# Kernel optimization log

Hardware: AMD Instinct MI355X
Metric: run time of the kernel (lower is better)

Reference implementation:

```python
import jax, jax.numpy as jnp
import numpy as np
from jax import lax

T, B = 80, 32
ACT, CIN, HID, LSTM_H = 16, 4, 512, 256

def _conv(x, w, b, stride, pad):
    y = lax.conv_general_dilated(x, w, (stride, stride), [(pad, pad), (pad, pad)],
                                 dimension_numbers=('NCHW', 'OIHW', 'NCHW'))
    return y + b[None, :, None, None]

def setup_inputs() -> dict:
    key = jax.random.key(0)
    ks = jax.random.split(key, 20)
    s = 0.02
    return {
        'x': jax.random.uniform(ks[0], (T, B, CIN, 84, 84), dtype=jnp.float32),
        'last_action': jax.random.randint(ks[1], (T, B), 0, ACT),
        'reward': jax.random.normal(ks[2], (T, B), dtype=jnp.float32),
        'dones': jnp.zeros((T, B), dtype=bool),
        'hx': jax.random.normal(ks[3], (2, B, LSTM_H), dtype=jnp.float32) * s,
        'conv1_w': jax.random.normal(ks[4], (32, CIN, 8, 8), jnp.float32) * s,
        'conv1_b': jnp.zeros((32,), jnp.float32),
        'conv2_w': jax.random.normal(ks[5], (64, 32, 4, 4), jnp.float32) * s,
        'conv2_b': jnp.zeros((64,), jnp.float32),
        'conv3_w': jax.random.normal(ks[6], (64, 64, 3, 3), jnp.float32) * s,
        'conv3_b': jnp.zeros((64,), jnp.float32),
        'fc_w': jax.random.normal(ks[7], (HID, 3136), jnp.float32) * s,
        'fc_b': jnp.zeros((HID,), jnp.float32),
        'lstm_wih': jax.random.normal(ks[8], (4 * LSTM_H, HID + ACT + 1), jnp.float32) * s,
        'lstm_whh': jax.random.normal(ks[9], (4 * LSTM_H, LSTM_H), jnp.float32) * s,
        'lstm_bih': jnp.zeros((4 * LSTM_H,), jnp.float32),
        'lstm_bhh': jnp.zeros((4 * LSTM_H,), jnp.float32),
        'actor_w': jax.random.normal(ks[10], (ACT, LSTM_H), jnp.float32) * s,
        'actor_b': jnp.zeros((ACT,), jnp.float32),
        'critic_w': jax.random.normal(ks[11], (1, LSTM_H), jnp.float32) * s,
        'critic_b': jnp.zeros((1,), jnp.float32),
    }

def reference(x, last_action, reward, dones, hx,
              conv1_w, conv1_b, conv2_w, conv2_b, conv3_w, conv3_b,
              fc_w, fc_b, lstm_wih, lstm_whh, lstm_bih, lstm_bhh,
              actor_w, actor_b, critic_w, critic_b):
    seq_len, bs = x.shape[0], x.shape[1]
    xf = x.reshape(seq_len * bs, CIN, 84, 84)          # combine time & batch
    la = jax.nn.one_hot(last_action.reshape(-1), ACT, dtype=jnp.float32)
    rw = reward.reshape(-1, 1)

    lrelu = lambda v: jax.nn.leaky_relu(v, 0.01)
    h = lrelu(_conv(xf, conv1_w, conv1_b, 4, 1))       # [N,32,20,20]
    h = lrelu(_conv(h, conv2_w, conv2_b, 2, 0))        # [N,64,9,9]
    h = lrelu(_conv(h, conv3_w, conv3_b, 1, 0))        # [N,64,7,7]
    h = h.reshape(h.shape[0], -1)                      # [N,3136]
    h = lrelu(h @ fc_w.T + fc_b)                       # [N,512]
    h = jnp.concatenate([h, rw, la], axis=1)           # [N,529]
    h = h.reshape(seq_len, bs, -1)

    def step(carry, inp):
        xt, dt = inp                                   # [bs,529], [bs] bool
        carry = jnp.where(dt[None, :, None], 0.0, carry)
        hh, cc = carry[0], carry[1]
        gates = xt @ lstm_wih.T + lstm_bih + hh @ lstm_whh.T + lstm_bhh
        i, f, g, o = jnp.split(gates, 4, axis=1)
        cc = jax.nn.sigmoid(f) * cc + jax.nn.sigmoid(i) * jnp.tanh(g)
        hh = jax.nn.sigmoid(o) * jnp.tanh(cc)
        return jnp.stack([hh, cc], 0), hh

    _, hs = lax.scan(step, hx, (h, dones))             # hs: [T,bs,256]
    feat = hs.reshape(seq_len * bs, LSTM_H)

    logits = feat @ actor_w.T + actor_b                # [N,16]
    values = feat @ critic_w.T + critic_b              # [N,1]
    logits = jnp.where(jnp.isnan(logits), jnp.float32(1e-12), logits)
    return logits.reshape(seq_len, -1, bs), values.reshape(seq_len, bs)
```

## Files before the change

kernel.cpp:

```cpp
#include <hip/hip_runtime.h>
#include <math.h>

#define T_ 80
#define B_ 32
#define N_ 2560
#define LH_ 256

typedef __attribute__((ext_vector_type(8))) short short8;
typedef __attribute__((ext_vector_type(4))) float f32x4;
#define MFMA16(a, b, c) __builtin_amdgcn_mfma_f32_16x16x32_bf16((a), (b), (c), 0, 0, 0)

__device__ __forceinline__ float lrelu(float v) { return v > 0.f ? v : 0.01f * v; }
__device__ __forceinline__ short f2bf(float f) {
    unsigned u = __float_as_uint(f);
    return (short)((u + 0x7fffu + ((u >> 16) & 1u)) >> 16);
}

__global__ void pack_all_k(const float* __restrict__ c1w, const float* __restrict__ c2w,
                           const float* __restrict__ c3w, const float* __restrict__ fcw,
                           const float* __restrict__ wih,
                           short* __restrict__ wp1, short* __restrict__ wp2,
                           short* __restrict__ wp3, short* __restrict__ wfcP,
                           short* __restrict__ wihP, int* __restrict__ cnt) {
    __shared__ short rowb[3136];
    int blk = blockIdx.x, tidx = threadIdx.x;
    if (blk < 512) {
        int j = blk;
        for (int i = tidx; i < 3136; i += 256) rowb[i] = f2bf(fcw[j * 3136 + i]);
        __syncthreads();
        for (int i = tidx; i < 3136; i += 256) {
            int p = i >> 6, oc = i & 63;
            wfcP[j * 3136 + i] = rowb[oc * 49 + p];
        }
        return;
    }
    blk -= 512;
    if (blk < 2048) {
        int g = blk * 256 + tidx;
        int r = g >> 9, k = g & 511;
        wihP[g] = f2bf(wih[r * 529 + k]);
        return;
    }
    blk -= 2048;
    if (blk < 32) {
        int g = blk * 256 + tidx;
        int ky = g >> 10, oc = (g >> 5) & 31, k = g & 31, kx = k >> 2, ci = k & 3;
        wp1[g] = f2bf(c1w[((oc * 4 + ci) * 8 + ky) * 8 + kx]);
        return;
    }
    blk -= 32;
    if (blk < 128) {
        int g = blk * 256 + tidx;
        int t = g >> 11, oc = (g >> 5) & 63, ci = g & 31, ky = t >> 2, kx = t & 3;
        wp2[g] = f2bf(c2w[((oc * 32 + ci) * 4 + ky) * 4 + kx]);
        return;
    }
    blk -= 128;
    if (blk < 144) {
        int g = blk * 256 + tidx;
        int tkc = g >> 11, oc = (g >> 5) & 63, c32 = g & 31;
        int t = tkc >> 1, kc = tkc & 1, ky = t / 3, kx = t % 3;
        wp3[g] = f2bf(c3w[((oc * 64 + kc * 32 + c32) * 3 + ky) * 3 + kx]);
        return;
    }
    cnt[tidx] = 0; cnt[256 + tidx] = 0;
}

#define C1_RS 344
__global__ __launch_bounds__(512) void conv123_mfma(
    const float* __restrict__ x,
    const short* __restrict__ wp1, const float* __restrict__ b1v,
    const short* __restrict__ wp2, const float* __restrict__ b2v,
    const short* __restrict__ wp3, const float* __restrict__ b3v,
    short* __restrict__ h3) {
    __shared__ short xs[44 * C1_RS];
    __shared__ short h1s[400 * 40];
    __shared__ short ob2[96 * 72];
    int n = blockIdx.x, tid = threadIdx.x;
    int lane = tid & 63, wid = tid >> 6;
    int lr = lane & 15, kq = lane >> 4;

    short8 bfr1[8][2];
#pragma unroll
    for (int ky = 0; ky < 8; ++ky)
#pragma unroll
        for (int nt = 0; nt < 2; ++nt)
            bfr1[ky][nt] = *(const short8*)&wp1[((ky * 32) + nt * 16 + lr) * 32 + kq * 8];
    float b0 = b1v[lr], b1 = b1v[16 + lr];

#pragma unroll
    for (int pass = 0; pass < 2; ++pass) {
        const int iybase = pass ? 39 : -1;
        for (int i = tid; i < 44 * 84; i += 512) {
            int ry = i / 84, xi4 = i % 84;
            int ci = xi4 / 21, x4 = xi4 % 21;
            int iy = iybase + ry;
            if (iy < 0) continue;
            float4 v = *(const float4*)(x + (size_t)(n * 4 + ci) * 7056 + iy * 84 + x4 * 4);
            int base = ry * C1_RS + (x4 * 4 + 1) * 4 + ci;
            xs[base] = f2bf(v.x); xs[base + 4] = f2bf(v.y);
            xs[base + 8] = f2bf(v.z); xs[base + 12] = f2bf(v.w);
        }
        for (int i = tid; i < 44 * 4; i += 512)
            xs[(i >> 2) * C1_RS + (i & 3)] = 0;
        if (pass == 0)
            for (int i = tid; i < C1_RS; i += 512) xs[i] = 0;
        __syncthreads();

        for (int t = wid; t < 13; t += 8) {
            int pl = t * 16 + lr; if (pl > 199) pl = 199;
            int p = pass * 200 + pl;
            int oy = p / 20, ox = p % 20;
            f32x4 acc0 = {0.f, 0.f, 0.f, 0.f}, acc1 = {0.f, 0.f, 0.f, 0.f};
#pragma unroll
            for (int ky = 0; ky < 8; ++ky) {
                int ry = oy * 4 + ky - (pass ? 40 : 0);
                short8 af = *(const short8*)&xs[ry * C1_RS + ox * 16 + kq * 8];
                acc0 = MFMA16(af, bfr1[ky][0], acc0);
                acc1 = MFMA16(af, bfr1[ky][1], acc1);
            }
#pragma unroll
            for (int r = 0; r < 4; ++r) {
                int rp = t * 16 + kq * 4 + r;
                if (rp < 200) {
                    int row = pass * 200 + rp;
                    h1s[row * 40 + lr]      = f2bf(lrelu(acc0[r] + b0));
                    h1s[row * 40 + 16 + lr] = f2bf(lrelu(acc1[r] + b1));
                }
            }
        }
        __syncthreads();
    }

    int nt = wid & 3, mh = wid >> 2;
    {
        short8 bfr[16];
#pragma unroll
        for (int t = 0; t < 16; ++t)
            bfr[t] = *(const short8*)&wp2[(t * 64 + nt * 16 + lr) * 32 + kq * 8];
        float bl = b2v[nt * 16 + lr];
        for (int mt = mh * 3; mt < mh * 3 + 3; ++mt) {
            int p = mt * 16 + lr; if (p > 80) p = 80;
            int oy = p / 9, ox = p % 9;
            f32x4 acc = {0.f, 0.f, 0.f, 0.f};
#pragma unroll
            for (int ky = 0; ky < 4; ++ky)
#pragma unroll
                for (int kx = 0; kx < 4; ++kx) {
                    int pix = (oy * 2 + ky) * 20 + ox * 2 + kx;
                    short8 af = *(const short8*)&h1s[pix * 40 + kq * 8];
                    acc = MFMA16(af, bfr[ky * 4 + kx], acc);
                }
            int pm = mt * 16 + kq * 4;
#pragma unroll
            for (int r = 0; r < 4; ++r)
                ob2[(pm + r) * 72 + nt * 16 + lr] = f2bf(lrelu(acc[r] + bl));
        }
    }
    __syncthreads();
    {
        short8 cfr[18];
#pragma unroll
        for (int t = 0; t < 18; ++t)
            cfr[t] = *(const short8*)&wp3[(t * 64 + nt * 16 + lr) * 32 + kq * 8];
        float bl3 = b3v[nt * 16 + lr];
        short* ob3 = xs;
        for (int mt = mh * 2; mt < mh * 2 + 2; ++mt) {
            int p = mt * 16 + lr; if (p > 48) p = 48;
            int oy = p / 7, ox = p % 7;
            f32x4 acc = {0.f, 0.f, 0.f, 0.f};
#pragma unroll
            for (int ky = 0; ky < 3; ++ky)
#pragma unroll
                for (int kx = 0; kx < 3; ++kx) {
                    int pix = (oy + ky) * 9 + ox + kx;
#pragma unroll
                    for (int kc = 0; kc < 2; ++kc) {
                        short8 af = *(const short8*)&ob2[pix * 72 + kc * 32 + kq * 8];
                        acc = MFMA16(af, cfr[(ky * 3 + kx) * 2 + kc], acc);
                    }
                }
            int pm = mt * 16 + kq * 4;
#pragma unroll
            for (int r = 0; r < 4; ++r)
                ob3[(pm + r) * 64 + nt * 16 + lr] = f2bf(lrelu(acc[r] + bl3));
        }
    }
    __syncthreads();
    uint4* dst = (uint4*)(h3 + (size_t)n * 3136);
    for (int i = tid; i < 392; i += 512) dst[i] = ((uint4*)xs)[i];
}

template <int OUT>
__global__ __launch_bounds__(256) void gemm_bf16(
    const short* __restrict__ A, const short* __restrict__ B,
    const float* __restrict__ bias, void* __restrict__ Cout,
    int M, int N, int K, int ldc,
    const float* __restrict__ reward = nullptr, const int* __restrict__ la = nullptr,
    const float* __restrict__ wih = nullptr, const float* __restrict__ bih = nullptr,
    const float* __restrict__ bhh = nullptr) {
    __shared__ short smem[15360];
    int m0 = blockIdx.y * 128, n0 = blockIdx.x * 64;
    int tid = threadIdx.x;
    int lane = tid & 63, wid = tid >> 6;
    int wr = wid >> 1, wc = wid & 1;
    int lr = lane & 15, kq = lane >> 4;
    f32x4 acc[4][2];
#pragma unroll
    for (int i = 0; i < 4; ++i)
#pragma unroll
        for (int j = 0; j < 2; ++j) acc[i][j] = (f32x4){0.f, 0.f, 0.f, 0.f};

    int nsteps = K >> 5;
#define STAGE(k0, buf)                                                          \
    {                                                                           \
        short* As = smem + (buf) * 5120;                                        \
        short* Bs = smem + 10240 + (buf) * 2560;                                \
        for (int i = tid; i < 512; i += 256) {                                  \
            int row = i >> 2, c4 = i & 3;                                       \
            *(uint4*)&As[row * 40 + c4 * 8] =                                   \
                *(const uint4*)&A[(size_t)(m0 + row) * K + (k0) + c4 * 8];      \
        }                                                                       \
        {                                                                       \
            int row = tid >> 2, c4 = tid & 3;                                   \
            *(uint4*)&Bs[row * 40 + c4 * 8] =                                   \
                *(const uint4*)&B[(size_t)(n0 + row) * K + (k0) + c4 * 8];      \
        }                                                                       \
    }
    STAGE(0, 0);
    __syncthreads();
    for (int ks = 0; ks < nsteps; ++ks) {
        int buf = ks & 1;
        if (ks + 1 < nsteps) STAGE((ks + 1) * 32, buf ^ 1);
        short* As = smem + buf * 5120;
        short* Bs = smem + 10240 + buf * 2560;
        short8 af[4], bfr[2];
#pragma unroll
        for (int i = 0; i < 4; ++i)
            af[i] = *(const short8*)&As[(wr * 64 + i * 16 + lr) * 40 + kq * 8];
#pragma unroll
        for (int j = 0; j < 2; ++j)
            bfr[j] = *(const short8*)&Bs[(wc * 32 + j * 16 + lr) * 40 + kq * 8];
#pragma unroll
        for (int i = 0; i < 4; ++i)
#pragma unroll
            for (int j = 0; j < 2; ++j)
                acc[i][j] = MFMA16(af[i], bfr[j], acc[i][j]);
        __syncthreads();
    }
#undef STAGE
    if (OUT == 2) {
        float* C = (float*)Cout;
#pragma unroll
        for (int i = 0; i < 4; ++i)
#pragma unroll
            for (int j = 0; j < 2; ++j) {
                int col = n0 + wc * 32 + j * 16 + lr;
                const float* wrow = wih + (size_t)col * 529;
                float base = bih[col] + bhh[col];
                float w512 = wrow[512];
#pragma unroll
                for (int r = 0; r < 4; ++r) {
                    int row = m0 + wr * 64 + i * 16 + kq * 4 + r;
                    C[(size_t)row * ldc + col] =
                        acc[i][j][r] + base + reward[row] * w512 + wrow[513 + la[row]];
                }
            }
    } else {
        short* ob = smem;
#pragma unroll
        for (int i = 0; i < 4; ++i)
#pragma unroll
            for (int j = 0; j < 2; ++j) {
                int col = wc * 32 + j * 16 + lr;
                float bl = bias[n0 + col];
#pragma unroll
                for (int r = 0; r < 4; ++r) {
                    int row = wr * 64 + i * 16 + kq * 4 + r;
                    ob[row * 64 + col] = f2bf(lrelu(acc[i][j][r] + bl));
                }
            }
        __syncthreads();
        short* C = (short*)Cout;
        for (int i = tid; i < 1024; i += 256) {
            int row = i >> 3, c8 = i & 7;
            *(uint4*)&C[(size_t)(m0 + row) * ldc + n0 + c8 * 8] =
                *(uint4*)&ob[row * 64 + c8 * 8];
        }
    }
}

__global__ __launch_bounds__(512) void lstm16_k(
    const float* __restrict__ gx,
    const float* __restrict__ whh,
    const unsigned char* __restrict__ dones,
    const float* __restrict__ hx,
    float* __restrict__ hs,
    unsigned short* __restrict__ hpub,
    int* __restrict__ cnt) {
    const int tid = threadIdx.x;
    const int grp  = blockIdx.x & 7;
    const int half = blockIdx.x >> 3;
    const int lane = tid & 63, w = tid >> 6;
    const int gt = w >> 1, s2 = w & 1;
    const int lr = lane & 15, kq = lane >> 4;

    __shared__ short hB[16 * 264];
    __shared__ float gate_s[4][128][4];

    short8 afr[4][8];
#pragma unroll
    for (int mi = 0; mi < 4; ++mi) {
        int row = gt * 256 + half * 128 + s2 * 64 + mi * 16 + lr;
        const float* wr = whh + (size_t)row * 256;
#pragma unroll
        for (int kt = 0; kt < 8; ++kt) {
            int k0 = kt * 32 + kq * 8;
            float4 a = *(const float4*)(wr + k0);
            float4 b = *(const float4*)(wr + k0 + 4);
            short8 f;
            f[0] = f2bf(a.x); f[1] = f2bf(a.y); f[2] = f2bf(a.z); f[3] = f2bf(a.w);
            f[4] = f2bf(b.x); f[5] = f2bf(b.y); f[6] = f2bf(b.z); f[7] = f2bf(b.w);
            afr[mi][kt] = f;
        }
    }
    {
        int* ap = (int*)afr;
#pragma unroll
        for (int i = 0; i < 128; ++i) asm volatile("" : "+v"(ap[i]));
    }

    for (int i = tid; i < 12 * 264; i += 512) hB[4 * 264 + i] = 0;

    const int u = tid >> 2, bt = tid & 3;
    const int b = grp * 4 + bt, gu = half * 128 + u;
    float cc = hx[(size_t)B_ * LH_ + b * LH_ + gu];

#pragma unroll
    for (int l = 0; l < 2; ++l) {
        int e = tid + l * 512;
        int bt2 = e >> 8, k = e & 255;
        int b2 = grp * 4 + bt2;
        float hv = hx[b2 * LH_ + k];
        if (dones[b2]) hv = 0.f;
        hB[bt2 * 264 + k] = f2bf(hv);
    }
    __syncthreads();

    const int mycnt = (grp * 2 + half) * 32, peercnt = (grp * 2 + (half ^ 1)) * 32;
    const int phalf = (half ^ 1) << 7;

    for (int t = 1; t <= T_; ++t) {
        const int nb0 = (t - 1) * B_;
        float gxv[4];
#pragma unroll
        for (int g2 = 0; g2 < 4; ++g2)
            gxv[g2] = gx[(size_t)(nb0 + b) * 1024 + g2 * 256 + gu];

        if (t > 1) {
            if (tid == 0) {
                while (__hip_atomic_load(&cnt[peercnt], __ATOMIC_RELAXED,
                                         __HIP_MEMORY_SCOPE_AGENT) < t - 1) {}
                __builtin_amdgcn_fence(__ATOMIC_ACQUIRE, "agent");
            }
            __syncthreads();
            int bt2 = tid >> 7, pu = tid & 127;
            int b2 = grp * 4 + bt2, pgu = phalf + pu;
            hB[bt2 * 264 + pgu] =
                (short)hpub[((t - 1) & 1) * 8192 + b2 * 256 + pgu];
        }
        __syncthreads();

        f32x4 acc[4] = {{0.f,0.f,0.f,0.f},{0.f,0.f,0.f,0.f},
                        {0.f,0.f,0.f,0.f},{0.f,0.f,0.f,0.f}};
#pragma unroll
        for (int kt = 0; kt < 8; ++kt) {
            short8 bfr = *(const short8*)&hB[lr * 264 + kt * 32 + kq * 8];
#pragma unroll
            for (int mi = 0; mi < 4; ++mi)
                acc[mi] = MFMA16(afr[mi][kt], bfr, acc[mi]);
        }
        if (lr < 4) {
#pragma unroll
            for (int mi = 0; mi < 4; ++mi)
#pragma unroll
                for (int r = 0; r < 4; ++r)
                    gate_s[gt][s2 * 64 + mi * 16 + kq * 4 + r][lr] = acc[mi][r];
        }
        __syncthreads();

        {
            bool dn = dones[nb0 + b] != 0;
            float gi = gate_s[0][u][bt] + gxv[0];
            float gf = gate_s[1][u][bt] + gxv[1];
            float gg = gate_s[2][u][bt] + gxv[2];
            float go = gate_s[3][u][bt] + gxv[3];
            float ccv = dn ? 0.f : cc;
            float si = 1.f / (1.f + expf(-gi));
            float sf = 1.f / (1.f + expf(-gf));
            float so = 1.f / (1.f + expf(-go));
            float c2 = sf * ccv + si * tanhf(gg);
            float h2 = so * tanhf(c2);
            cc = c2;
            if (t < T_) {
                short hm = f2bf(dones[t * B_ + b] ? 0.f : h2);
                hpub[(t & 1) * 8192 + b * 256 + gu] = (unsigned short)hm;
                hB[bt * 264 + gu] = hm;
            }
            hs[(size_t)(nb0 + b) * LH_ + gu] = h2;
        }
        __syncthreads();
        if (tid == 0)
            __hip_atomic_store(&cnt[mycnt], t, __ATOMIC_RELEASE,
                               __HIP_MEMORY_SCOPE_AGENT);
    }
}

__global__ void head_k(const float* __restrict__ hs,
                       const float* __restrict__ aw, const float* __restrict__ ab,
                       const float* __restrict__ cw, const float* __restrict__ cb,
                       float* __restrict__ out) {
    int gid = blockIdx.x * 256 + threadIdx.x;
    if (gid >= N_ * 17) return;
    int n = gid / 17, r = gid % 17;
    const float* f = hs + (size_t)n * 256;
    if (r < 16) {
        const float* w = aw + r * 256;
        float acc = ab[r];
        for (int k = 0; k < 256; ++k) acc = fmaf(f[k], w[k], acc);
        if (isnan(acc)) acc = 1e-12f;
        out[(size_t)n * 16 + r] = acc;
    } else {
        float acc = cb[0];
        for (int k = 0; k < 256; ++k) acc = fmaf(f[k], cw[k], acc);
        out[(size_t)N_ * 16 + n] = acc;
    }
}

extern "C" void kernel_launch(void* const* d_in, const int* in_sizes, int n_in,
                              void* d_out, int out_size, void* d_ws, size_t ws_size,
                              hipStream_t stream) {
    const float* x      = (const float*)d_in[0];
    const int* la       = (const int*)d_in[1];
    const float* reward = (const float*)d_in[2];
    const unsigned char* dones = (const unsigned char*)d_in[3];
    const float* hx     = (const float*)d_in[4];
    const float* c1w = (const float*)d_in[5];  const float* c1b = (const float*)d_in[6];
    const float* c2w = (const float*)d_in[7];  const float* c2b = (const float*)d_in[8];
    const float* c3w = (const float*)d_in[9];  const float* c3b = (const float*)d_in[10];
    const float* fcw = (const float*)d_in[11]; const float* fcb = (const float*)d_in[12];
    const float* wih = (const float*)d_in[13]; const float* whh = (const float*)d_in[14];
    const float* bih = (const float*)d_in[15]; const float* bhh = (const float*)d_in[16];
    const float* aw  = (const float*)d_in[17]; const float* ab  = (const float*)d_in[18];
    const float* cw  = (const float*)d_in[19]; const float* cb  = (const float*)d_in[20];

    char* wsb = (char*)d_ws;
    short* h3   = (short*)(wsb + 92078080);
    short* hfc  = (short*)(wsb + 108134400);
    float* gx   = (float*)(wsb + 110755840);
    float* hs   = (float*)(wsb + 121241600);
    unsigned short* hpub = (unsigned short*)(wsb + 123863040);
    int*   cnt  = (int*)  (wsb + 123928576);
    short* wp1  = (short*)(wsb + 123932672);
    short* wp2  = (short*)(wsb + 123949056);
    short* wp3  = (short*)(wsb + 124014592);
    short* wfcP = (short*)(wsb + 124088320);
    short* wihP = (short*)(wsb + 127299584);

    pack_all_k<<<2865, 256, 0, stream>>>(c1w, c2w, c3w, fcw, wih,
                                         wp1, wp2, wp3, wfcP, wihP, cnt);

    conv123_mfma<<<2560, 512, 0, stream>>>(x, wp1, c1b, wp2, c2b, wp3, c3b, h3);

    gemm_bf16<1><<<dim3(8, 20), 256, 0, stream>>>(h3, wfcP, fcb, hfc,
                                                  2560, 512, 3136, 512);
    gemm_bf16<2><<<dim3(16, 20), 256, 0, stream>>>(hfc, wihP, nullptr, gx,
                                                   2560, 1024, 512, 1024,
                                                   reward, la, wih, bih, bhh);

    lstm16_k<<<16, 512, 0, stream>>>(gx, whh, dones, hx, hs, hpub, cnt);
    head_k<<<170, 256, 0, stream>>>(hs, aw, ab, cw, cb, (float*)d_out);
}
```

Before: 482.0 us.

## Make each LSTM block own full hidden state for two batches, drop cross-block sync

Before, pairs of blocks split the hidden units and swapped half-states every timestep through global memory with atomic counters and spin-waits. Now each of 16 blocks handles 2 batch elements across all 256 hidden units, so the recurrence needs no inter-block communication. The full recurrent weight matrix is held per block: 6 of 8 row tiles per wave stay in registers and the rest sit in 128KB of LDS. This removes the global handoff latency each step. In exchange, each block does twice the MFMA work with mostly idle batch columns, and register and LDS pressure rise.

```diff
diff --git a/kernel.cpp b/kernel.cpp
--- a/kernel.cpp
+++ b/kernel.cpp
@@ -21,7 +21,7 @@
                            const float* __restrict__ wih,
                            short* __restrict__ wp1, short* __restrict__ wp2,
                            short* __restrict__ wp3, short* __restrict__ wfcP,
-                           short* __restrict__ wihP, int* __restrict__ cnt) {
+                           short* __restrict__ wihP) {
     __shared__ short rowb[3136];
     int blk = blockIdx.x, tidx = threadIdx.x;
     if (blk < 512) {
@@ -56,14 +56,12 @@
         return;
     }
     blk -= 128;
-    if (blk < 144) {
+    {
         int g = blk * 256 + tidx;
         int tkc = g >> 11, oc = (g >> 5) & 63, c32 = g & 31;
         int t = tkc >> 1, kc = tkc & 1, ky = t / 3, kx = t % 3;
         wp3[g] = f2bf(c3w[((oc * 64 + kc * 32 + c32) * 3 + ky) * 3 + kx]);
-        return;
-    }
-    cnt[tidx] = 0; cnt[256 + tidx] = 0;
+    }
 }
 
 #define C1_RS 344
@@ -290,34 +288,31 @@
     }
 }
 
-__global__ __launch_bounds__(512) void lstm16_k(
+__global__ __launch_bounds__(512, 2) void lstm_bs_k(
     const float* __restrict__ gx,
     const float* __restrict__ whh,
     const unsigned char* __restrict__ dones,
     const float* __restrict__ hx,
-    float* __restrict__ hs,
-    unsigned short* __restrict__ hpub,
-    int* __restrict__ cnt) {
+    float* __restrict__ hs) {
     const int tid = threadIdx.x;
-    const int grp  = blockIdx.x & 7;
-    const int half = blockIdx.x >> 3;
+    const int g2 = blockIdx.x;
     const int lane = tid & 63, w = tid >> 6;
-    const int gt = w >> 1, s2 = w & 1;
     const int lr = lane & 15, kq = lane >> 4;
 
+    __shared__ short wL[65536];
     __shared__ short hB[16 * 264];
-    __shared__ float gate_s[4][128][4];
-
-    short8 afr[4][8];
-#pragma unroll
-    for (int mi = 0; mi < 4; ++mi) {
-        int row = gt * 256 + half * 128 + s2 * 64 + mi * 16 + lr;
-        const float* wr = whh + (size_t)row * 256;
+    __shared__ float gate_s[4 * 256 * 2];
+
+    short8 afr[6][8];
+#pragma unroll
+    for (int mi = 0; mi < 6; ++mi) {
+        int row = w * 128 + mi * 16 + lr;
+        const float* wrp = whh + (size_t)row * 256;
 #pragma unroll
         for (int kt = 0; kt < 8; ++kt) {
             int k0 = kt * 32 + kq * 8;
-            float4 a = *(const float4*)(wr + k0);
-            float4 b = *(const float4*)(wr + k0 + 4);
+            float4 a = *(const float4*)(wrp + k0);
+            float4 b = *(const float4*)(wrp + k0 + 4);
             short8 f;
             f[0] = f2bf(a.x); f[1] = f2bf(a.y); f[2] = f2bf(a.z); f[3] = f2bf(a.w);
             f[4] = f2bf(b.x); f[5] = f2bf(b.y); f[6] = f2bf(b.z); f[7] = f2bf(b.w);
@@ -327,74 +322,74 @@
     {
         int* ap = (int*)afr;
 #pragma unroll
-        for (int i = 0; i < 128; ++i) asm volatile("" : "+v"(ap[i]));
-    }
-
-    for (int i = tid; i < 12 * 264; i += 512) hB[4 * 264 + i] = 0;
-
-    const int u = tid >> 2, bt = tid & 3;
-    const int b = grp * 4 + bt, gu = half * 128 + u;
-    float cc = hx[(size_t)B_ * LH_ + b * LH_ + gu];
-
-#pragma unroll
-    for (int l = 0; l < 2; ++l) {
-        int e = tid + l * 512;
-        int bt2 = e >> 8, k = e & 255;
-        int b2 = grp * 4 + bt2;
+        for (int i = 0; i < 192; ++i) asm volatile("" : "+v"(ap[i]));
+    }
+
+    for (int s = tid; s < 8192; s += 512) {
+        int w2 = s >> 10, m2 = (s >> 9) & 1, kt = (s >> 6) & 7, ln = s & 63;
+        int row = w2 * 128 + (6 + m2) * 16 + (ln & 15);
+        int k0 = kt * 32 + (ln >> 4) * 8;
+        const float* wrp = whh + (size_t)row * 256 + k0;
+        short8 f;
+#pragma unroll
+        for (int e = 0; e < 8; ++e) f[e] = f2bf(wrp[e]);
+        *(short8*)&wL[s * 8] = f;
+    }
+
+    for (int i = tid; i < 14 * 264; i += 512) hB[2 * 264 + i] = 0;
+
+    const int u = tid >> 1, bt = tid & 1;
+    const int b = g2 * 2 + bt;
+    float cc = hx[(size_t)B_ * LH_ + b * LH_ + u];
+
+    {
+        int bt2 = tid >> 8, k = tid & 255;
+        int b2 = g2 * 2 + bt2;
         float hv = hx[b2 * LH_ + k];
         if (dones[b2]) hv = 0.f;
         hB[bt2 * 264 + k] = f2bf(hv);
     }
     __syncthreads();
 
-    const int mycnt = (grp * 2 + half) * 32, peercnt = (grp * 2 + (half ^ 1)) * 32;
-    const int phalf = (half ^ 1) << 7;
-
     for (int t = 1; t <= T_; ++t) {
         const int nb0 = (t - 1) * B_;
         float gxv[4];
 #pragma unroll
-        for (int g2 = 0; g2 < 4; ++g2)
-            gxv[g2] = gx[(size_t)(nb0 + b) * 1024 + g2 * 256 + gu];
-
-        if (t > 1) {
-            if (tid == 0) {
-                while (__hip_atomic_load(&cnt[peercnt], __ATOMIC_RELAXED,
-                                         __HIP_MEMORY_SCOPE_AGENT) < t - 1) {}
-                __builtin_amdgcn_fence(__ATOMIC_ACQUIRE, "agent");
-            }
-            __syncthreads();
-            int bt2 = tid >> 7, pu = tid & 127;
-            int b2 = grp * 4 + bt2, pgu = phalf + pu;
-            hB[bt2 * 264 + pgu] =
-                (short)hpub[((t - 1) & 1) * 8192 + b2 * 256 + pgu];
-        }
-        __syncthreads();
-
-        f32x4 acc[4] = {{0.f,0.f,0.f,0.f},{0.f,0.f,0.f,0.f},
-                        {0.f,0.f,0.f,0.f},{0.f,0.f,0.f,0.f}};
+        for (int gg2 = 0; gg2 < 4; ++gg2)
+            gxv[gg2] = gx[(size_t)(nb0 + b) * 1024 + gg2 * 256 + u];
+
+        f32x4 acc[8];
+#pragma unroll
+        for (int mi = 0; mi < 8; ++mi) acc[mi] = (f32x4){0.f, 0.f, 0.f, 0.f};
 #pragma unroll
         for (int kt = 0; kt < 8; ++kt) {
             short8 bfr = *(const short8*)&hB[lr * 264 + kt * 32 + kq * 8];
 #pragma unroll
-            for (int mi = 0; mi < 4; ++mi)
+            for (int mi = 0; mi < 6; ++mi)
                 acc[mi] = MFMA16(afr[mi][kt], bfr, acc[mi]);
-        }
-        if (lr < 4) {
-#pragma unroll
-            for (int mi = 0; mi < 4; ++mi)
-#pragma unroll
-                for (int r = 0; r < 4; ++r)
-                    gate_s[gt][s2 * 64 + mi * 16 + kq * 4 + r][lr] = acc[mi][r];
+#pragma unroll
+            for (int m2 = 0; m2 < 2; ++m2) {
+                short8 lA = *(const short8*)&wL[(((w * 2 + m2) * 8 + kt) * 64 + lane) * 8];
+                acc[6 + m2] = MFMA16(lA, bfr, acc[6 + m2]);
+            }
+        }
+        if (lr < 2) {
+#pragma unroll
+            for (int mi = 0; mi < 8; ++mi)
+#pragma unroll
+                for (int r = 0; r < 4; ++r) {
+                    int row = w * 128 + mi * 16 + kq * 4 + r;
+                    gate_s[(row >> 8) * 512 + (row & 255) * 2 + lr] = acc[mi][r];
+                }
         }
         __syncthreads();
 
         {
             bool dn = dones[nb0 + b] != 0;
-            float gi = gate_s[0][u][bt] + gxv[0];
-            float gf = gate_s[1][u][bt] + gxv[1];
-            float gg = gate_s[2][u][bt] + gxv[2];
-            float go = gate_s[3][u][bt] + gxv[3];
+            float gi = gate_s[0 * 512 + u * 2 + bt] + gxv[0];
+            float gf = gate_s[1 * 512 + u * 2 + bt] + gxv[1];
+            float gg = gate_s[2 * 512 + u * 2 + bt] + gxv[2];
+            float go = gate_s[3 * 512 + u * 2 + bt] + gxv[3];
             float ccv = dn ? 0.f : cc;
             float si = 1.f / (1.f + expf(-gi));
             float sf = 1.f / (1.f + expf(-gf));
@@ -403,16 +398,11 @@
             float h2 = so * tanhf(c2);
             cc = c2;
             if (t < T_) {
-                short hm = f2bf(dones[t * B_ + b] ? 0.f : h2);
-                hpub[(t & 1) * 8192 + b * 256 + gu] = (unsigned short)hm;
-                hB[bt * 264 + gu] = hm;
-            }
-            hs[(size_t)(nb0 + b) * LH_ + gu] = h2;
-        }
-        __syncthreads();
-        if (tid == 0)
-            __hip_atomic_store(&cnt[mycnt], t, __ATOMIC_RELEASE,
-                               __HIP_MEMORY_SCOPE_AGENT);
+                hB[bt * 264 + u] = f2bf(dones[t * B_ + b] ? 0.f : h2);
+            }
+            hs[(size_t)(nb0 + b) * LH_ + u] = h2;
+        }
+        __syncthreads();
     }
 }
 
@@ -459,16 +449,14 @@
     short* hfc  = (short*)(wsb + 108134400);
     float* gx   = (float*)(wsb + 110755840);
     float* hs   = (float*)(wsb + 121241600);
-    unsigned short* hpub = (unsigned short*)(wsb + 123863040);
-    int*   cnt  = (int*)  (wsb + 123928576);
     short* wp1  = (short*)(wsb + 123932672);
     short* wp2  = (short*)(wsb + 123949056);
     short* wp3  = (short*)(wsb + 124014592);
     short* wfcP = (short*)(wsb + 124088320);
     short* wihP = (short*)(wsb + 127299584);
 
-    pack_all_k<<<2865, 256, 0, stream>>>(c1w, c2w, c3w, fcw, wih,
-                                         wp1, wp2, wp3, wfcP, wihP, cnt);
+    pack_all_k<<<2864, 256, 0, stream>>>(c1w, c2w, c3w, fcw, wih,
+                                         wp1, wp2, wp3, wfcP, wihP);
 
     conv123_mfma<<<2560, 512, 0, stream>>>(x, wp1, c1b, wp2, c2b, wp3, c3b, h3);
 
@@ -478,6 +466,6 @@
                                                    2560, 1024, 512, 1024,
                                                    reward, la, wih, bih, bhh);
 
-    lstm16_k<<<16, 512, 0, stream>>>(gx, whh, dones, hx, hs, hpub, cnt);
+    lstm_bs_k<<<16, 512, 0, stream>>>(gx, whh, dones, hx, hs);
     head_k<<<170, 256, 0, stream>>>(hs, aw, ab, cw, cb, (float*)d_out);
 }
```

New measurement: 468.1 us, median of 2. 2.9% less time.
